# Kernel optimization log

Hardware: AMD Instinct MI355X
Metric: run time of the kernel (lower is better)

Reference implementation:

```python
import jax, jax.numpy as jnp
import numpy as np

TEMPERATURE = 10000.0
LN_EPS = 1e-5

def build_freqs(H, W, head_dim):
    # (H*W, head_dim) rotary angles: [theta_h, theta_h, theta_w, theta_w]
    gh, gw = jnp.meshgrid(jnp.arange(H, dtype=jnp.float32), jnp.arange(W, dtype=jnp.float32), indexing='ij')
    dq = head_dim // 4
    freq = 1.0 / (TEMPERATURE ** (jnp.arange(dq, dtype=jnp.float32) / dq))
    th = gh.reshape(-1, 1) * freq[None, :]
    tw = gw.reshape(-1, 1) * freq[None, :]
    return jnp.concatenate([th, th, tw, tw], axis=-1)

def apply_rope(x, freqs):
    # x: (B, nh, N, hd), freqs: (N, hd)
    cos = jnp.cos(freqs)[None, None]
    sin = jnp.sin(freqs)[None, None]
    hd = x.shape[-1]
    x1, x2 = x[..., :hd // 2], x[..., hd // 2:]
    x_rot = jnp.concatenate([-x2, x1], axis=-1)
    return x * cos + x_rot * sin

def setup_inputs() -> dict:
    key = jax.random.key(0)
    ks = jax.random.split(key, 8)
    dim, hidden, B, H, W = 192, 384, 4, 128, 128
    N = H * W
    s = 0.02
    return {
        'x': jax.random.normal(ks[0], (B, N, dim), jnp.float32),
        'in_w': jax.random.normal(ks[1], (hidden, dim), jnp.float32) * s,
        'in_b': jnp.zeros((hidden,), jnp.float32),
        'qkv_w': jax.random.normal(ks[2], (3 * hidden, hidden), jnp.float32) * s,
        'qkv_b': jnp.zeros((3 * hidden,), jnp.float32),
        'lepe_w': jax.random.normal(ks[3], (hidden, 1, 3, 3), jnp.float32) * s,
        'lepe_b': jnp.zeros((hidden,), jnp.float32),
        'ln_g': jnp.ones((hidden,), jnp.float32),
        'ln_b': jnp.zeros((hidden,), jnp.float32),
        'out_w': jax.random.normal(ks[4], (dim, hidden), jnp.float32) * s,
        'out_b': jnp.zeros((dim,), jnp.float32),
        'H': H,
        'W': W,
    }

def reference(x, in_w, in_b, qkv_w, qkv_b, lepe_w, lepe_b, ln_g, ln_b, out_w, out_b, H, W):
    B, N, C = x.shape
    hidden = in_w.shape[0]
    nh = 8
    hd = hidden // nh
    # in_proj: 1x1 conv == per-token linear
    x_seq = jnp.einsum('bnc,hc->bnh', x, in_w) + in_b
    # fused qkv
    qkv = jnp.einsum('bnh,oh->bno', x_seq, qkv_w) + qkv_b
    q, k, v = jnp.split(qkv, 3, axis=-1)
    # LEPE: 3x3 depthwise conv on V in NCHW layout
    v2d = v.transpose(0, 2, 1).reshape(B, hidden, H, W)
    lepe = jax.lax.conv_general_dilated(
        v2d, lepe_w, window_strides=(1, 1), padding=((1, 1), (1, 1)),
        feature_group_count=hidden, dimension_numbers=('NCHW', 'OIHW', 'NCHW'))
    lepe = lepe + lepe_b[None, :, None, None]
    v = v + lepe.reshape(B, hidden, N).transpose(0, 2, 1)
    # split heads -> (B, nh, N, hd)
    q = q.reshape(B, N, nh, hd).transpose(0, 2, 1, 3)
    k = k.reshape(B, N, nh, hd).transpose(0, 2, 1, 3)
    v = v.reshape(B, N, nh, hd).transpose(0, 2, 1, 3)
    freqs = build_freqs(H, W, hd)
    q = apply_rope(q, freqs)
    k = apply_rope(k, freqs)
    # phi = ELU + 1 feature map
    q = jax.nn.elu(q) + 1.0
    k = jax.nn.elu(k) + 1.0
    # linear attention associativity trick
    kv = jnp.einsum('bhnd,bhne->bhde', k, v)
    out = jnp.einsum('bhnd,bhde->bhne', q, kv)
    k_sum = k.sum(axis=2)  # (B, nh, hd)
    denom = jnp.maximum(jnp.einsum('bhnd,bhd->bhn', q, k_sum)[..., None], 1e-6)
    out = out / denom
    out = out.transpose(0, 2, 1, 3).reshape(B, N, hidden)
    # LayerNorm + out_proj
    mu = out.mean(axis=-1, keepdims=True)
    var = out.var(axis=-1, keepdims=True)
    out = (out - mu) * jax.lax.rsqrt(var + LN_EPS) * ln_g + ln_b
    return jnp.einsum('bnh,ch->bnc', out, out_w) + out_b
```

## Files before the change

### kernel.cpp

```cpp
#include <hip/hip_runtime.h>
#include <cstdint>
#include <cstddef>

#define NN_TOK 16384
#define ROWS   65536
#define CDIM   192
#define HID    384
#define NHEAD  8
#define HD     48
#define QKVO   1152

typedef unsigned short ushort_t;
typedef __bf16 bf16x8 __attribute__((ext_vector_type(8)));
typedef float  f32x4  __attribute__((ext_vector_type(4)));

__device__ __forceinline__ ushort_t f2bf(float f) {
  unsigned int u = __float_as_uint(f);
  u += 0x7fffu + ((u >> 16) & 1u);
  return (ushort_t)(u >> 16);
}
__device__ __forceinline__ float bf2f(ushort_t u) {
  return __uint_as_float(((unsigned int)u) << 16);
}

__global__ void cast_x(const float* __restrict__ x, ushort_t* __restrict__ xb, int n8) {
  int i = blockIdx.x * blockDim.x + threadIdx.x;
  if (i >= n8) return;
  const float4* src = (const float4*)(x + (size_t)i * 8);
  float4 f0 = src[0], f1 = src[1];
  uint4 pk;
  pk.x = (unsigned)f2bf(f0.x) | ((unsigned)f2bf(f0.y) << 16);
  pk.y = (unsigned)f2bf(f0.z) | ((unsigned)f2bf(f0.w) << 16);
  pk.z = (unsigned)f2bf(f1.x) | ((unsigned)f2bf(f1.y) << 16);
  pk.w = (unsigned)f2bf(f1.z) | ((unsigned)f2bf(f1.w) << 16);
  *(uint4*)(xb + (size_t)i * 8) = pk;
}

__global__ void combine_w(const float* __restrict__ in_w, const float* __restrict__ in_b,
                          const float* __restrict__ qkv_w, const float* __restrict__ qkv_b,
                          ushort_t* __restrict__ Wcb, float* __restrict__ bc) {
  int o = blockIdx.x;
  int c = threadIdx.x;
  const float* qw = qkv_w + o * HID;
  float s = 0.f;
  for (int m = 0; m < HID; ++m) s += qw[m] * in_w[m * CDIM + c];
  Wcb[o * CDIM + c] = f2bf(s);
  if (c == 0) {
    float sb = qkv_b[o];
    for (int m = 0; m < HID; ++m) sb += qw[m] * in_b[m];
    bc[o] = sb;
  }
}

__global__ void cast_ow(const float* __restrict__ w, ushort_t* __restrict__ wb, int n) {
  int i = blockIdx.x * blockDim.x + threadIdx.x;
  if (i < n) wb[i] = f2bf(w[i]);
}

__global__ void build_tab(float4* __restrict__ tab4) {
  int i = blockIdx.x * blockDim.x + threadIdx.x;
  if (i >= NN_TOK * 24) return;
  int n = i / 24, dp = i - n * 24;
  int j = dp % 12;
  const float c0 = 1.1073093649624542f;
  float freq = exp2f(-(float)j * c0);
  float fy = (float)(n >> 7), fx = (float)(n & 127);
  float s1, c1, s2, c2;
  sincosf(fy * freq, &s1, &c1);
  sincosf(fx * freq, &s2, &c2);
  tab4[i] = make_float4(c1, s1, c2, s2);
}

template<int BM, int BN, int WM, int WN, bool OUTBF16>
__global__ __launch_bounds__(256) void gemm_mfma(const ushort_t* __restrict__ A, int lda,
                                                 const ushort_t* __restrict__ Wb,
                                                 const float* __restrict__ bias,
                                                 void* __restrict__ Cptr,
                                                 int K, int O, int nbx) {
  constexpr int TM = BM / WM / 16;
  constexpr int TN = BN / WN / 16;
  __shared__ __align__(16) ushort_t As[BM][40];
  __shared__ __align__(16) ushort_t Bs[BN][40];
  const int t    = threadIdx.x;
  const int lane = t & 63;
  const int wave = t >> 6;
  const int quad = lane >> 4;
  const int l15  = lane & 15;
  const int wm   = wave / WN, wn = wave % WN;
  const int m_base = wm * (BM / WM);
  const int n_base = wn * (BN / WN);
  const int cpx = gridDim.x >> 3;
  const int id  = blockIdx.x;
  const int swz = (id & 7) * cpx + (id >> 3);
  const int o0  = (swz % nbx) * BN;
  const int n0  = (swz / nbx) * BM;
  f32x4 acc[TM][TN] = {};

  for (int kt = 0; kt < K; kt += 32) {
    for (int c = t; c < BM * 4; c += 256) {
      int row = c >> 2, col8 = (c & 3) * 8;
      *(uint4*)&As[row][col8] = *(const uint4*)(A + (size_t)(n0 + row) * lda + kt + col8);
    }
    for (int c = t; c < BN * 4; c += 256) {
      int row = c >> 2, col8 = (c & 3) * 8;
      *(uint4*)&Bs[row][col8] = *(const uint4*)(Wb + (size_t)(o0 + row) * K + kt + col8);
    }
    __syncthreads();
    bf16x8 af[TM], bfr[TN];
#pragma unroll
    for (int mi = 0; mi < TM; ++mi)
      af[mi] = *(const bf16x8*)&As[m_base + mi * 16 + l15][quad * 8];
#pragma unroll
    for (int ni = 0; ni < TN; ++ni)
      bfr[ni] = *(const bf16x8*)&Bs[n_base + ni * 16 + l15][quad * 8];
#pragma unroll
    for (int mi = 0; mi < TM; ++mi)
#pragma unroll
      for (int ni = 0; ni < TN; ++ni)
        acc[mi][ni] = __builtin_amdgcn_mfma_f32_16x16x32_bf16(af[mi], bfr[ni], acc[mi][ni], 0, 0, 0);
    __syncthreads();
  }
#pragma unroll
  for (int mi = 0; mi < TM; ++mi) {
#pragma unroll
    for (int ni = 0; ni < TN; ++ni) {
      int col = o0 + n_base + ni * 16 + l15;
      float bv = bias[col];
      int rbase = n0 + m_base + mi * 16 + quad * 4;
#pragma unroll
      for (int r = 0; r < 4; ++r) {
        float val = acc[mi][ni][r] + bv;
        if (OUTBF16) ((ushort_t*)Cptr)[(size_t)(rbase + r) * O + col] = f2bf(val);
        else         ((float*)Cptr)[(size_t)(rbase + r) * O + col] = val;
      }
    }
  }
}

__global__ __launch_bounds__(256) void kv_partial_k(const ushort_t* __restrict__ kq,
                                                    const ushort_t* __restrict__ vq,
                                                    const float4* __restrict__ tab4,
                                                    const float* __restrict__ lw,
                                                    const float* __restrict__ lb,
                                                    float* __restrict__ part) {
  const int bid   = blockIdx.x;
  const int chunk = bid & 63;
  const int bh    = bid >> 6;
  const int b     = bh >> 3;
  const int h     = bh & 7;
  const int t     = threadIdx.x;
  const int lane  = t & 63;
  const int wave  = t >> 6;
  __shared__ __align__(16) ushort_t ksF[3][16][16][8];
  __shared__ __align__(16) ushort_t vsF[3][16][16][8];
  __shared__ float wlds[9][48];
  __shared__ float blds[48];
  float* red   = (float*)&ksF[0][0][0][0];
  float* ksred = (float*)&vsF[0][0][0][0];
  for (int c = t; c < 432; c += 256) {
    int ch = c / 9, tap = c - ch * 9;
    wlds[tap][ch] = lw[(h * HD + ch) * 9 + tap];
  }
  if (t < 48) blds[t] = lb[h * HD + t];
  __syncthreads();

  const int g  = lane >> 4;
  const int d0 = lane & 15;
  f32x4 acc[3][3] = {};
  float ksacc = 0.f;
  const int n0 = b * NN_TOK + chunk * 256;

  for (int it = 0; it < 2; ++it) {
    const int nbase = it * 128;
    for (int c = t; c < 384; c += 256) {
      int rr = c / 3, s8 = (c - (c / 3) * 3) * 8;
      int n  = n0 + nbase + rr;
      int nn = n & (NN_TOK - 1);
      const ushort_t* kr = kq + (size_t)n * QKVO + h * HD;
      uint4 ka = *(const uint4*)(kr + s8);
      uint4 kb = *(const uint4*)(kr + s8 + 24);
      ushort_t ua[8], ub[8];
      *(uint4*)ua = ka; *(uint4*)ub = kb;
      const float4* t4 = tab4 + nn * 24 + s8;
      const int nb = rr >> 3, nm = rr & 7;
#pragma unroll
      for (int jj = 0; jj < 8; ++jj) {
        float4 cs = t4[jj];
        float in1 = bf2f(ua[jj]), in2 = bf2f(ub[jj]);
        float o1 = in1 * cs.x - in2 * cs.y;
        float o2 = in2 * cs.z + in1 * cs.w;
        o1 = (o1 > 0.f) ? o1 + 1.f : expf(o1);
        o2 = (o2 > 0.f) ? o2 + 1.f : expf(o2);
        const int d1 = s8 + jj, d2 = s8 + 24 + jj;
        ksF[d1 >> 4][nb][d1 & 15][nm] = f2bf(o1);
        ksF[d2 >> 4][nb][d2 & 15][nm] = f2bf(o2);
      }
    }
    {
      const int nst = chunk * 256 + nbase;
      const int y   = nst >> 7;
      for (int c = t; c < 768; c += 256) {
        int rr = c / 6, gg = c - (c / 6) * 6;
        int x = rr;
        float a8[8], ctr[8];
#pragma unroll
        for (int ci = 0; ci < 8; ++ci) a8[ci] = blds[gg * 8 + ci];
#pragma unroll
        for (int dy = -1; dy <= 1; ++dy) {
#pragma unroll
          for (int dx = -1; dx <= 1; ++dx) {
            int yy = y + dy, xx = x + dx;
            float m = ((unsigned)yy < 128u && (unsigned)xx < 128u) ? 1.f : 0.f;
            int yc = min(max(yy, 0), 127), xc = min(max(xx, 0), 127);
            const ushort_t* src = vq + ((size_t)(b * NN_TOK + (yc << 7) + xc)) * QKVO + h * HD + gg * 8;
            uint4 pk = *(const uint4*)src;
            ushort_t uu[8];
            *(uint4*)uu = pk;
            const int tap = (dy + 1) * 3 + (dx + 1);
#pragma unroll
            for (int ci = 0; ci < 8; ++ci) {
              float val = bf2f(uu[ci]);
              if (dy == 0 && dx == 0) ctr[ci] = val;
              a8[ci] += (wlds[tap][gg * 8 + ci] * m) * val;
            }
          }
        }
        const int nb = rr >> 3, nm = rr & 7;
#pragma unroll
        for (int ci = 0; ci < 8; ++ci) {
          const int e = gg * 8 + ci;
          vsF[e >> 4][nb][e & 15][nm] = f2bf(ctr[ci] + a8[ci]);
        }
      }
    }
    __syncthreads();
    {
      const int w4 = wave * 4 + g;
      bf16x8 af[3], bfr[3];
#pragma unroll
      for (int dg = 0; dg < 3; ++dg) af[dg]  = *(const bf16x8*)&ksF[dg][w4][d0][0];
#pragma unroll
      for (int eg = 0; eg < 3; ++eg) bfr[eg] = *(const bf16x8*)&vsF[eg][w4][d0][0];
#pragma unroll
      for (int dg = 0; dg < 3; ++dg)
#pragma unroll
        for (int eg = 0; eg < 3; ++eg)
          acc[dg][eg] = __builtin_amdgcn_mfma_f32_16x16x32_bf16(af[dg], bfr[eg], acc[dg][eg], 0, 0, 0);
    }
    if (lane < 48) {
      const int dg = lane >> 4, dd = lane & 15;
#pragma unroll 8
      for (int rr = 0; rr < 32; ++rr) {
        int nl = wave * 32 + rr;
        ksacc += bf2f(ksF[dg][nl >> 3][dd][nl & 7]);
      }
    }
    __syncthreads();
  }
  if (wave == 0) {
#pragma unroll
    for (int dg = 0; dg < 3; ++dg)
#pragma unroll
      for (int eg = 0; eg < 3; ++eg)
#pragma unroll
        for (int r = 0; r < 4; ++r)
          red[(dg * 16 + g * 4 + r) * 48 + eg * 16 + d0] = acc[dg][eg][r];
  }
  if (lane < 48) ksred[wave * 48 + lane] = ksacc;
  __syncthreads();
  for (int w = 1; w < 4; ++w) {
    if (wave == w) {
#pragma unroll
      for (int dg = 0; dg < 3; ++dg)
#pragma unroll
        for (int eg = 0; eg < 3; ++eg)
#pragma unroll
          for (int r = 0; r < 4; ++r)
            red[(dg * 16 + g * 4 + r) * 48 + eg * 16 + d0] += acc[dg][eg][r];
    }
    __syncthreads();
  }
  float* p = part + (size_t)bid * 2352;
  for (int c = t; c < 2304; c += 256) p[c] = red[c];
  if (t < 48) p[2304 + t] = ksred[t] + ksred[48 + t] + ksred[96 + t] + ksred[144 + t];
}

__global__ void kv_phase2(const float* __restrict__ part, ushort_t* __restrict__ kvT) {
  int bh  = blockIdx.x >> 3;
  int seg = blockIdx.x & 7;
  int t   = threadIdx.x;
  ushort_t* dst = kvT + (size_t)bh * 8192;
  for (int i = seg * 1024 + t; i < (seg + 1) * 1024; i += 256) {
    int rem = i & 4095, e = rem >> 6, d = rem & 63;
    if (d >= 48 || e >= 49) dst[i] = 0;
  }
  int cend = (seg + 1) * 294;
  for (int c = seg * 294 + t; c < cend; c += 256) {
    const float* p = part + (size_t)(bh * 64) * 2352 + c;
    float s = 0.f;
    for (int ch = 0; ch < 64; ++ch) s += p[(size_t)ch * 2352];
    int d, e;
    if (c < 2304) { d = c / 48; e = c - d * 48; }
    else          { e = 48; d = c - 2304; }
    ushort_t hi = f2bf(s);
    float lo = s - bf2f(hi);
    dst[(size_t)e * 64 + d]        = hi;
    dst[4096 + (size_t)e * 64 + d] = f2bf(lo);
  }
}

__global__ __launch_bounds__(256) void attn_ln_fused(const ushort_t* __restrict__ q,
                                                     const float4* __restrict__ tab4,
                                                     const ushort_t* __restrict__ kvT,
                                                     const float* __restrict__ ln_g,
                                                     const float* __restrict__ ln_b,
                                                     ushort_t* __restrict__ oln) {
  __shared__ __align__(16) ushort_t qsL[32][392];
  __shared__ float lnp[4][32][2];
  const int t    = threadIdx.x;
  const int lane = t & 63;
  const int wave = t >> 6;
  const int quad = lane >> 4;
  const int l15  = lane & 15;
  const int row0 = blockIdx.x * 32;
  const int b    = row0 >> 14;
  const int h0   = wave * 2;
  const float2* tab2 = (const float2*)tab4;

  for (int c = t; c < 1536; c += 256) {
    int r = c / 48, seg = c - (c / 48) * 48;
    *(uint4*)&qsL[r][seg * 8] = *(const uint4*)(q + (size_t)(row0 + r) * QKVO + seg * 8);
  }
  __syncthreads();

  f32x4 acc[2][2][4] = {};

  float gg[2][3], bb[2][3];
#pragma unroll
  for (int hi = 0; hi < 2; ++hi)
#pragma unroll
    for (int nt = 0; nt < 3; ++nt) {
      int col = (h0 + hi) * 48 + nt * 16 + l15;
      gg[hi][nt] = ln_g[col];
      bb[hi][nt] = ln_b[col];
    }

#pragma unroll
  for (int s = 0; s < 2; ++s) {
    const int d0 = s * 32 + quad * 8;
    const bool valid = d0 < 48;
    const bool caseA = d0 < 24;
    const int dp0 = caseA ? d0 : d0 - 24;
    bf16x8 af[2][2] = {};
    if (valid) {
      const int dpart = caseA ? d0 + 24 : d0 - 24;
      const int csel  = caseA ? 0 : 1;
      const float sgn = caseA ? -1.f : 1.f;
#pragma unroll
      for (int m = 0; m < 2; ++m) {
        const int r  = row0 + m * 16 + l15;
        const int nn = r & (NN_TOK - 1);
        float2 cs[8];
#pragma unroll
        for (int j = 0; j < 8; ++j) cs[j] = tab2[(size_t)(nn * 24 + dp0 + j) * 2 + csel];
#pragma unroll
        for (int hi = 0; hi < 2; ++hi) {
          const ushort_t* qr = &qsL[m * 16 + l15][(h0 + hi) * 48];
          uint4 pr = *(const uint4*)(qr + d0);
          uint4 pa = *(const uint4*)(qr + dpart);
          ushort_t up[8], ua[8];
          *(uint4*)up = pr; *(uint4*)ua = pa;
          unsigned w[4];
#pragma unroll
          for (int j2 = 0; j2 < 4; ++j2) {
            float o2[2];
#pragma unroll
            for (int k = 0; k < 2; ++k) {
              int j = j2 * 2 + k;
              float vp = bf2f(up[j]), va = bf2f(ua[j]);
              float o = vp * cs[j].x + va * (sgn * cs[j].y);
              o2[k] = (o > 0.f) ? o + 1.f : expf(o);
            }
            w[j2] = (unsigned)f2bf(o2[0]) | ((unsigned)f2bf(o2[1]) << 16);
          }
          uint4 pk = make_uint4(w[0], w[1], w[2], w[3]);
          af[hi][m] = *(bf16x8*)&pk;
        }
      }
    }
#pragma unroll
    for (int hi = 0; hi < 2; ++hi) {
      const ushort_t* kb = kvT + (size_t)(b * 8 + h0 + hi) * 8192;
#pragma unroll
      for (int nt = 0; nt < 4; ++nt) {
        bf16x8 bH = *(const bf16x8*)(kb + (nt * 16 + l15) * 64 + d0);
        bf16x8 bL = *(const bf16x8*)(kb + 4096 + (nt * 16 + l15) * 64 + d0);
#pragma unroll
        for (int m = 0; m < 2; ++m) {
          acc[hi][m][nt] = __builtin_amdgcn_mfma_f32_16x16x32_bf16(af[hi][m], bH, acc[hi][m][nt], 0, 0, 0);
          acc[hi][m][nt] = __builtin_amdgcn_mfma_f32_16x16x32_bf16(af[hi][m], bL, acc[hi][m][nt], 0, 0, 0);
        }
      }
    }
  }

  float rdn[2][2][4];
#pragma unroll
  for (int hi = 0; hi < 2; ++hi)
#pragma unroll
    for (int m = 0; m < 2; ++m)
#pragma unroll
      for (int r = 0; r < 4; ++r) {
        float dn = __shfl(acc[hi][m][3][r], lane & 48);
        rdn[hi][m][r] = 1.f / fmaxf(dn, 1e-6f);
      }
  float s1[2][4] = {}, s2[2][4] = {};
#pragma unroll
  for (int hi = 0; hi < 2; ++hi)
#pragma unroll
    for (int m = 0; m < 2; ++m)
#pragma unroll
      for (int nt = 0; nt < 3; ++nt)
#pragma unroll
        for (int r = 0; r < 4; ++r) {
          float o = acc[hi][m][nt][r] * rdn[hi][m][r];
          acc[hi][m][nt][r] = o;
          s1[m][r] += o;
          s2[m][r] += o * o;
        }
#pragma unroll
  for (int m = 0; m < 2; ++m)
#pragma unroll
    for (int r = 0; r < 4; ++r) {
#pragma unroll
      for (int msk = 1; msk < 16; msk <<= 1) {
        s1[m][r] += __shfl_xor(s1[m][r], msk, 64);
        s2[m][r] += __shfl_xor(s2[m][r], msk, 64);
      }
    }
  if (l15 == 0) {
#pragma unroll
    for (int m = 0; m < 2; ++m)
#pragma unroll
      for (int r = 0; r < 4; ++r) {
        int rr = m * 16 + quad * 4 + r;
        lnp[wave][rr][0] = s1[m][r];
        lnp[wave][rr][1] = s2[m][r];
      }
  }
  __syncthreads();
  float muv[2][4], rsv[2][4];
#pragma unroll
  for (int m = 0; m < 2; ++m)
#pragma unroll
    for (int r = 0; r < 4; ++r) {
      int rr = m * 16 + quad * 4 + r;
      float a  = lnp[0][rr][0] + lnp[1][rr][0] + lnp[2][rr][0] + lnp[3][rr][0];
      float bq = lnp[0][rr][1] + lnp[1][rr][1] + lnp[2][rr][1] + lnp[3][rr][1];
      float mu  = a * (1.f / 384.f);
      float var = bq * (1.f / 384.f) - mu * mu;
      muv[m][r] = mu;
      rsv[m][r] = rsqrtf(var + 1e-5f);
    }
#pragma unroll
  for (int hi = 0; hi < 2; ++hi)
#pragma unroll
    for (int m = 0; m < 2; ++m)
#pragma unroll
      for (int nt = 0; nt < 3; ++nt) {
        int col = (h0 + hi) * 48 + nt * 16 + l15;
#pragma unroll
        for (int r = 0; r < 4; ++r) {
          int rr = m * 16 + quad * 4 + r;
          float v = (acc[hi][m][nt][r] - muv[m][r]) * rsv[m][r] * gg[hi][nt] + bb[hi][nt];
          qsL[rr][col] = f2bf(v);
        }
      }
  __syncthreads();
  for (int c = t; c < 1536; c += 256) {
    int r = c / 48, seg = c - (c / 48) * 48;
    *(uint4*)(oln + (size_t)(row0 + r) * QKVO + seg * 8) = *(const uint4*)&qsL[r][seg * 8];
  }
}

extern "C" void kernel_launch(void* const* d_in, const int* in_sizes, int n_in,
                              void* d_out, int out_size, void* d_ws, size_t ws_size,
                              hipStream_t stream) {
  const float* x      = (const float*)d_in[0];
  const float* in_w   = (const float*)d_in[1];
  const float* in_b   = (const float*)d_in[2];
  const float* qkv_w  = (const float*)d_in[3];
  const float* qkv_b  = (const float*)d_in[4];
  const float* lepe_w = (const float*)d_in[5];
  const float* lepe_b = (const float*)d_in[6];
  const float* ln_g   = (const float*)d_in[7];
  const float* ln_b   = (const float*)d_in[8];
  const float* out_w  = (const float*)d_in[9];
  const float* out_b  = (const float*)d_in[10];
  float* out = (float*)d_out;

  float*    ws     = (float*)d_ws;
  float*    qkvbF  = ws;
  float*    xbF    = qkvbF + (size_t)ROWS * QKVO / 2;
  float*    WcbF   = xbF   + (size_t)ROWS * CDIM / 2;
  float*    bc     = WcbF  + (size_t)QKVO * CDIM / 2;
  float*    owbF   = bc    + QKVO;
  float*    tab4F  = owbF  + (size_t)CDIM * HID / 2;
  ushort_t* qkvb   = (ushort_t*)qkvbF;
  ushort_t* xb     = (ushort_t*)xbF;
  float*    part   = xbF;
  ushort_t* kvT    = (ushort_t*)(xbF + (size_t)2048 * 2352);
  ushort_t* Wcb    = (ushort_t*)WcbF;
  ushort_t* owb    = (ushort_t*)owbF;
  float4*   tab4   = (float4*)tab4F;

  cast_x<<<(ROWS * CDIM / 8 + 255) / 256, 256, 0, stream>>>(x, xb, ROWS * CDIM / 8);
  combine_w<<<QKVO, CDIM, 0, stream>>>(in_w, in_b, qkv_w, qkv_b, Wcb, bc);
  cast_ow<<<(CDIM * HID + 255) / 256, 256, 0, stream>>>(out_w, owb, CDIM * HID);
  build_tab<<<(NN_TOK * 24 + 255) / 256, 256, 0, stream>>>(tab4);

  gemm_mfma<128, 128, 2, 2, true><<<4608, 256, 0, stream>>>(
      xb, CDIM, Wcb, bc, qkvb, CDIM, QKVO, 9);

  kv_partial_k<<<2048, 256, 0, stream>>>(qkvb + HID, qkvb + 2 * HID, tab4, lepe_w, lepe_b, part);
  kv_phase2<<<256, 256, 0, stream>>>(part, kvT);

  attn_ln_fused<<<ROWS / 32, 256, 0, stream>>>(qkvb, tab4, kvT, ln_g, ln_b, qkvb + HID);

  gemm_mfma<128, 64, 4, 1, false><<<1536, 256, 0, stream>>>(
      qkvb + HID, QKVO, owb, out_b, out, HID, CDIM, 3);
}
```

Before: 412.6 us.

## Fold k_sum into MFMA via ones column and pad LDS fragment layout

The k-sum reduction is now computed by the matrix cores: a fourth V fragment group is filled with a ones column (bf16 1.0 at dd==0), so the extra MFMA output column gives sum_n k, and the scalar LDS summation loop and its separate reduction buffer are removed. The LDS fragment arrays get a padded stride (136 per nb, 2200 per group), likely to reduce bank conflicts. The LEPE boundary mask now zeroes the loaded vector instead of multiplying weights, and weights and bias are read as float4. The cost is three extra MFMAs per iteration, a larger reduction buffer, and a 49-column packing into the partials with divisions.

```diff
diff --git a/kernel.cpp b/kernel.cpp
--- a/kernel.cpp
+++ b/kernel.cpp
@@ -137,6 +137,10 @@
   }
 }
 
+__device__ __forceinline__ int fragEl(int pg, int nb, int dd, int nm) {
+  return pg * 2200 + nb * 136 + dd * 8 + nm;
+}
+
 __global__ __launch_bounds__(256) void kv_partial_k(const ushort_t* __restrict__ kq,
                                                     const ushort_t* __restrict__ vq,
                                                     const float4* __restrict__ tab4,
@@ -151,23 +155,25 @@
   const int t     = threadIdx.x;
   const int lane  = t & 63;
   const int wave  = t >> 6;
-  __shared__ __align__(16) ushort_t ksF[3][16][16][8];
-  __shared__ __align__(16) ushort_t vsF[3][16][16][8];
-  __shared__ float wlds[9][48];
-  __shared__ float blds[48];
-  float* red   = (float*)&ksF[0][0][0][0];
-  float* ksred = (float*)&vsF[0][0][0][0];
+  __shared__ __align__(16) ushort_t ksR[3 * 2200];
+  __shared__ __align__(16) ushort_t vsR[4 * 2200];
+  __shared__ __align__(16) float wlds[9][48];
+  __shared__ __align__(16) float blds[48];
+  float* red = (float*)&ksR[0];
   for (int c = t; c < 432; c += 256) {
     int ch = c / 9, tap = c - ch * 9;
     wlds[tap][ch] = lw[(h * HD + ch) * 9 + tap];
   }
   if (t < 48) blds[t] = lb[h * HD + t];
+  for (int c = t; c < 2048; c += 256) {
+    int nb = c >> 7, dd = (c >> 3) & 15, nm = c & 7;
+    vsR[fragEl(3, nb, dd, nm)] = (dd == 0) ? (ushort_t)0x3F80 : (ushort_t)0;
+  }
   __syncthreads();
 
   const int g  = lane >> 4;
   const int d0 = lane & 15;
-  f32x4 acc[3][3] = {};
-  float ksacc = 0.f;
+  f32x4 acc[3][4] = {};
   const int n0 = b * NN_TOK + chunk * 256;
 
   for (int it = 0; it < 2; ++it) {
@@ -192,8 +198,8 @@
         o1 = (o1 > 0.f) ? o1 + 1.f : expf(o1);
         o2 = (o2 > 0.f) ? o2 + 1.f : expf(o2);
         const int d1 = s8 + jj, d2 = s8 + 24 + jj;
-        ksF[d1 >> 4][nb][d1 & 15][nm] = f2bf(o1);
-        ksF[d2 >> 4][nb][d2 & 15][nm] = f2bf(o2);
+        ksR[fragEl(d1 >> 4, nb, d1 & 15, nm)] = f2bf(o1);
+        ksR[fragEl(d2 >> 4, nb, d2 & 15, nm)] = f2bf(o2);
       }
     }
     {
@@ -203,25 +209,29 @@
         int rr = c / 6, gg = c - (c / 6) * 6;
         int x = rr;
         float a8[8], ctr[8];
-#pragma unroll
-        for (int ci = 0; ci < 8; ++ci) a8[ci] = blds[gg * 8 + ci];
+        *(float4*)&a8[0] = *(const float4*)&blds[gg * 8];
+        *(float4*)&a8[4] = *(const float4*)&blds[gg * 8 + 4];
 #pragma unroll
         for (int dy = -1; dy <= 1; ++dy) {
 #pragma unroll
           for (int dx = -1; dx <= 1; ++dx) {
             int yy = y + dy, xx = x + dx;
-            float m = ((unsigned)yy < 128u && (unsigned)xx < 128u) ? 1.f : 0.f;
+            bool inb = ((unsigned)yy < 128u) && ((unsigned)xx < 128u);
             int yc = min(max(yy, 0), 127), xc = min(max(xx, 0), 127);
             const ushort_t* src = vq + ((size_t)(b * NN_TOK + (yc << 7) + xc)) * QKVO + h * HD + gg * 8;
             uint4 pk = *(const uint4*)src;
+            if (!inb) pk = make_uint4(0u, 0u, 0u, 0u);
+            const int tap = (dy + 1) * 3 + (dx + 1);
+            float wt[8];
+            *(float4*)&wt[0] = *(const float4*)&wlds[tap][gg * 8];
+            *(float4*)&wt[4] = *(const float4*)&wlds[tap][gg * 8 + 4];
             ushort_t uu[8];
             *(uint4*)uu = pk;
-            const int tap = (dy + 1) * 3 + (dx + 1);
 #pragma unroll
             for (int ci = 0; ci < 8; ++ci) {
               float val = bf2f(uu[ci]);
               if (dy == 0 && dx == 0) ctr[ci] = val;
-              a8[ci] += (wlds[tap][gg * 8 + ci] * m) * val;
+              a8[ci] += wt[ci] * val;
             }
           }
         }
@@ -229,60 +239,53 @@
 #pragma unroll
         for (int ci = 0; ci < 8; ++ci) {
           const int e = gg * 8 + ci;
-          vsF[e >> 4][nb][e & 15][nm] = f2bf(ctr[ci] + a8[ci]);
+          vsR[fragEl(e >> 4, nb, e & 15, nm)] = f2bf(ctr[ci] + a8[ci]);
         }
       }
     }
     __syncthreads();
     {
       const int w4 = wave * 4 + g;
-      bf16x8 af[3], bfr[3];
-#pragma unroll
-      for (int dg = 0; dg < 3; ++dg) af[dg]  = *(const bf16x8*)&ksF[dg][w4][d0][0];
-#pragma unroll
-      for (int eg = 0; eg < 3; ++eg) bfr[eg] = *(const bf16x8*)&vsF[eg][w4][d0][0];
+      bf16x8 af[3], bfr[4];
+#pragma unroll
+      for (int dg = 0; dg < 3; ++dg) af[dg]  = *(const bf16x8*)&ksR[fragEl(dg, w4, d0, 0)];
+#pragma unroll
+      for (int eg = 0; eg < 4; ++eg) bfr[eg] = *(const bf16x8*)&vsR[fragEl(eg, w4, d0, 0)];
 #pragma unroll
       for (int dg = 0; dg < 3; ++dg)
 #pragma unroll
-        for (int eg = 0; eg < 3; ++eg)
+        for (int eg = 0; eg < 4; ++eg)
           acc[dg][eg] = __builtin_amdgcn_mfma_f32_16x16x32_bf16(af[dg], bfr[eg], acc[dg][eg], 0, 0, 0);
     }
-    if (lane < 48) {
-      const int dg = lane >> 4, dd = lane & 15;
-#pragma unroll 8
-      for (int rr = 0; rr < 32; ++rr) {
-        int nl = wave * 32 + rr;
-        ksacc += bf2f(ksF[dg][nl >> 3][dd][nl & 7]);
-      }
-    }
     __syncthreads();
   }
   if (wave == 0) {
 #pragma unroll
     for (int dg = 0; dg < 3; ++dg)
 #pragma unroll
-      for (int eg = 0; eg < 3; ++eg)
+      for (int eg = 0; eg < 4; ++eg)
 #pragma unroll
         for (int r = 0; r < 4; ++r)
-          red[(dg * 16 + g * 4 + r) * 48 + eg * 16 + d0] = acc[dg][eg][r];
-  }
-  if (lane < 48) ksred[wave * 48 + lane] = ksacc;
+          red[(dg * 16 + g * 4 + r) * 64 + eg * 16 + d0] = acc[dg][eg][r];
+  }
   __syncthreads();
   for (int w = 1; w < 4; ++w) {
     if (wave == w) {
 #pragma unroll
       for (int dg = 0; dg < 3; ++dg)
 #pragma unroll
-        for (int eg = 0; eg < 3; ++eg)
+        for (int eg = 0; eg < 4; ++eg)
 #pragma unroll
           for (int r = 0; r < 4; ++r)
-            red[(dg * 16 + g * 4 + r) * 48 + eg * 16 + d0] += acc[dg][eg][r];
+            red[(dg * 16 + g * 4 + r) * 64 + eg * 16 + d0] += acc[dg][eg][r];
     }
     __syncthreads();
   }
   float* p = part + (size_t)bid * 2352;
-  for (int c = t; c < 2304; c += 256) p[c] = red[c];
-  if (t < 48) p[2304 + t] = ksred[t] + ksred[48 + t] + ksred[96 + t] + ksred[144 + t];
+  for (int c = t; c < 2352; c += 256) {
+    int d = c / 49, e = c - d * 49;
+    p[c] = red[d * 64 + e];
+  }
 }
 
 __global__ void kv_phase2(const float* __restrict__ part, ushort_t* __restrict__ kvT) {
@@ -299,9 +302,7 @@
     const float* p = part + (size_t)(bh * 64) * 2352 + c;
     float s = 0.f;
     for (int ch = 0; ch < 64; ++ch) s += p[(size_t)ch * 2352];
-    int d, e;
-    if (c < 2304) { d = c / 48; e = c - d * 48; }
-    else          { e = 48; d = c - 2304; }
+    int d = c / 49, e = c - d * 49;
     ushort_t hi = f2bf(s);
     float lo = s - bf2f(hi);
     dst[(size_t)e * 64 + d]        = hi;
```

Result: no change. 416.0 us (+0.8%).
